# Optimization experiments

Measured on AMD Instinct MI355X. Metric: run time of the kernel, lower is better.

The kernel has to match this reference:

```python
import jax, jax.numpy as jnp
import numpy as np

B, C, H, W = 8, 256, 32, 32
N_HEAD, D_K, D_V, OUT_C = 8, 32, 32, 256


def _relative_indices(height, width):
    # idx[i, j] = (y_j - y_i + H) * W + (x_j - x_i + W), matching the torch loop
    ys, xs = np.meshgrid(np.arange(height), np.arange(width), indexing='ij')
    ys, xs = ys.reshape(-1), xs.reshape(-1)  # [L]
    rel_y = ys[None, :] - ys[:, None] + height  # [L, L]
    rel_x = xs[None, :] - xs[:, None] + width
    return jnp.asarray(rel_y * width + rel_x, dtype=jnp.int32)


def setup_inputs() -> dict:
    key = jax.random.key(0)
    ks = jax.random.split(key, 7)
    sc = lambda fan_in: 1.0 / np.sqrt(fan_in)
    table = ((2 * H - 1) * (2 * W - 1))  # 3969
    return {
        'x': jax.random.normal(ks[0], (B, C, H, W), jnp.float32),
        'Qw': jax.random.normal(ks[1], (C, N_HEAD * D_K), jnp.float32) * sc(C),
        'Kw': jax.random.normal(ks[2], (C, N_HEAD * D_K), jnp.float32) * sc(C),
        'Vw': jax.random.normal(ks[3], (C, N_HEAD * D_V), jnp.float32) * sc(C),
        'ffw': jax.random.normal(ks[4], (N_HEAD * D_V, OUT_C), jnp.float32) * sc(N_HEAD * D_V),
        'ffb': jax.random.normal(ks[5], (OUT_C,), jnp.float32) * 0.01,
        'rel_bias': jax.random.normal(ks[6], (N_HEAD, table), jnp.float32),
        'rel_idx': _relative_indices(H, W),  # [L, L] int32
    }


def reference(x, Qw, Kw, Vw, ffw, ffb, rel_bias, rel_idx):
    b, c, h_, w_ = x.shape
    L = h_ * w_
    nh = rel_bias.shape[0]
    dk = Qw.shape[1] // nh
    dv = Vw.shape[1] // nh
    xf = x.reshape(b, c, L).transpose(0, 2, 1)  # [b, L, c]
    q = (xf @ Qw).reshape(b, L, nh, dk).transpose(0, 2, 1, 3)  # [b, h, L, dk]
    k = (xf @ Kw).reshape(b, L, nh, dk).transpose(0, 2, 1, 3)
    v = (xf @ Vw).reshape(b, L, nh, dv).transpose(0, 2, 1, 3)
    bias = rel_bias[:, rel_idx]  # gather -> [h, L, L]
    sim = jnp.einsum('bhid,bhjd->bhij', q, k) + bias[None]  # no 1/sqrt(dk) in original
    attn = jax.nn.softmax(sim, axis=-1)  # dropout is identity in eval
    out = jnp.einsum('bhij,bhjd->bhid', attn, v)  # [b, h, L, dv]
    out = out.transpose(0, 2, 1, 3).reshape(b, L, nh * dv)
    out = out @ ffw + ffb  # [b, L, out_c]
    return out.transpose(0, 2, 1).reshape(b, -1, h_, w_)
```

## Files before the change

### kernel.cpp

```cpp
#include <hip/hip_runtime.h>
#include <math.h>


typedef unsigned short u16;
typedef __bf16 bf16;
typedef bf16 bf16x8 __attribute__((ext_vector_type(8)));
typedef bf16 bf16x4 __attribute__((ext_vector_type(4)));
typedef short s16x4 __attribute__((ext_vector_type(4)));
typedef float f32x4 __attribute__((ext_vector_type(4)));
typedef float f32x4u __attribute__((ext_vector_type(4), aligned(4)));
typedef u16 u16x8 __attribute__((ext_vector_type(8)));
typedef u16 u16x4 __attribute__((ext_vector_type(4)));

#define DEVI __device__ __forceinline__

DEVI u16 bfbits(float f) { return __builtin_bit_cast(u16, (bf16)f); }

DEVI void async_cp16(const u16* g, u16* l) {
    __builtin_amdgcn_global_load_lds((const __attribute__((address_space(1))) void*)g,
                                     (__attribute__((address_space(3))) void*)l, 16, 0, 0);
}

DEVI f32x4 pv_mfma(bf16x4 a, bf16x4 b, f32x4 c) {
#if __has_builtin(__builtin_amdgcn_mfma_f32_16x16x16bf16_1k)
    return __builtin_amdgcn_mfma_f32_16x16x16bf16_1k(
        __builtin_bit_cast(s16x4, a), __builtin_bit_cast(s16x4, b), c, 0, 0, 0);
#else
    asm("s_nop 1\n\tv_mfma_f32_16x16x16_bf16 %0, %1, %2, %0"
        : "+v"(c) : "v"(a), "v"(b));
    return c;
#endif
}

__global__ __launch_bounds__(256) void prep(const float* __restrict__ X,
                                            const float* __restrict__ Qw, const float* __restrict__ Kw,
                                            const float* __restrict__ Vw, const float* __restrict__ Fw,
                                            const float* __restrict__ RB,
                                            u16* __restrict__ XF, u16* __restrict__ WT,
                                            float* __restrict__ RBs) {
    __shared__ u16 t[64 * 65];
    const int blk = blockIdx.x, tid = threadIdx.x;
    if (blk < 576) {
        const float* src;
        int cbase, rbase, rows_total;
        u16* dst;
        if (blk < 512) {
            const int b = blk >> 6;
            cbase = (blk & 3) * 64; rbase = ((blk >> 2) & 15) * 64;
            src = X + (size_t)b * 256 * 1024; dst = XF + (size_t)b * 1024 * 256;
            rows_total = 1024;
        } else {
            const int t2 = blk - 512, wsel = t2 >> 4;
            cbase = (t2 & 3) * 64; rbase = ((t2 >> 2) & 3) * 64;
            src = wsel == 0 ? Qw : wsel == 1 ? Kw : wsel == 2 ? Vw : Fw;
            dst = WT + (size_t)wsel * 256 * 256;
            rows_total = 256;
        }
        const int w = tid >> 6, r = tid & 63;
#pragma unroll
        for (int i = 0; i < 16; i++) {
            const int c = w * 16 + i;
            t[c * 65 + r] = bfbits(src[(size_t)(cbase + c) * rows_total + rbase + r]);
        }
        __syncthreads();
#pragma unroll
        for (int i = 0; i < 2; i++) {
            const int idx = i * 256 + tid;
            const int r2 = idx >> 3, cg = idx & 7;
            u16x8 v;
#pragma unroll
            for (int j = 0; j < 8; j++) v[j] = t[(cg * 8 + j) * 65 + r2];
            *(u16x8*)&dst[(size_t)(rbase + r2) * 256 + cbase + cg * 8] = v;
        }
    } else {
        const int n = 8 * 3969;
        for (int i = (blk - 576) * 256 + tid; i < n; i += 32 * 256)
            RBs[i] = RB[i] * 1.44269504f;
    }
}

__global__ __launch_bounds__(256, 6) void gemm_fused(const u16* __restrict__ xf, const u16* __restrict__ wt,
                                                     u16* __restrict__ q, u16* __restrict__ kk,
                                                     u16* __restrict__ vt, const u16* __restrict__ ob,
                                                     float* __restrict__ outf, const float* __restrict__ ffb,
                                                     int base_mode) {
    __shared__ __align__(16) u16 lA[64 * 32];
    __shared__ __align__(16) u16 lB[64 * 32];
    const int tid = threadIdx.x;
    const int wave = tid >> 6, lane = tid & 63;
    const int quad = lane >> 4, l15 = lane & 15;

    int mode, mbase, nbase;
    const u16 *A, *Bt;
    if (base_mode == 2) {
        mode = 2; A = wt + 768 * 256; Bt = ob;
        mbase = (blockIdx.x & 3) * 64; nbase = (blockIdx.x >> 2) * 64;
    } else if (blockIdx.x < 1024) {
        mode = 0; A = xf; Bt = wt;
        mbase = (blockIdx.x >> 3) * 64; nbase = (blockIdx.x & 7) * 64;
    } else {
        mode = 1; A = wt + 512 * 256; Bt = xf;
        const int t = blockIdx.x - 1024;
        mbase = (t & 3) * 64; nbase = (t >> 2) * 64;
    }

    const int m0 = (wave >> 1) * 32, n0 = (wave & 1) * 32;
    const int srow = tid >> 2;
    const int sgcol = (lane & 3) ^ ((lane >> 3) & 3);
    const size_t arow = (size_t)(mbase + srow) * 256 + sgcol * 8;
    const size_t brow = (size_t)(nbase + srow) * 256 + sgcol * 8;
    const int kcol = ((quad ^ ((l15 >> 1) & 3))) * 8;

    f32x4 acc[2][2];
#pragma unroll
    for (int i = 0; i < 2; i++)
#pragma unroll
        for (int j = 0; j < 2; j++) acc[i][j] = f32x4{0.f, 0.f, 0.f, 0.f};

    for (int kb = 0; kb < 256; kb += 32) {
        __syncthreads();
        async_cp16(&A[arow + kb], &lA[wave * 512]);
        async_cp16(&Bt[brow + kb], &lB[wave * 512]);
        __syncthreads();
        bf16x8 af[2], bfr[2];
#pragma unroll
        for (int i = 0; i < 2; i++) af[i] = *(const bf16x8*)&lA[(m0 + i * 16 + l15) * 32 + kcol];
#pragma unroll
        for (int j = 0; j < 2; j++) bfr[j] = *(const bf16x8*)&lB[(n0 + j * 16 + l15) * 32 + kcol];
#pragma unroll
        for (int i = 0; i < 2; i++)
#pragma unroll
            for (int j = 0; j < 2; j++)
                acc[i][j] = __builtin_amdgcn_mfma_f32_16x16x32_bf16(af[i], bfr[j], acc[i][j], 0, 0, 0);
    }

#pragma unroll
    for (int i = 0; i < 2; i++) {
#pragma unroll
        for (int j = 0; j < 2; j++) {
#pragma unroll
            for (int r = 0; r < 4; r++) {
                const int gm = mbase + m0 + i * 16 + quad * 4 + r;
                const int gn = nbase + n0 + j * 16 + l15;
                float v = acc[i][j][r];
                if (mode == 0) {
                    const int b = gm >> 10, l = gm & 1023;
                    int n = gn;
                    u16* dst = q;
                    if (n >= 256) { n -= 256; dst = kk; }
                    else v *= 1.44269504f;
                    const int h = n >> 5, d = n & 31;
                    dst[(((size_t)(b * 8 + h) * 1024 + l) << 5) + d] = bfbits(v);
                } else if (mode == 1) {
                    const int h = gm >> 5, d = gm & 31;
                    const int b = gn >> 10, l = gn & 1023;
                    vt[(((size_t)(b * 8 + h) * 32 + d) << 10) + l] = bfbits(v);
                } else {
                    const int b = gn >> 10, l = gn & 1023;
                    outf[(((size_t)(b * 256 + gm)) << 10) + l] = v + ffb[gm];
                }
            }
        }
    }
}

__global__ __launch_bounds__(256, 4) void attn(const u16* __restrict__ Q, const u16* __restrict__ Kb,
                                               const u16* __restrict__ Vt, const float* __restrict__ RBs,
                                               u16* __restrict__ O) {
    __shared__ __align__(16) u16 kbuf[4][2][32 * 32];
    __shared__ __align__(16) u16 vbuf[4][2][32 * 32];
    const int tid = threadIdx.x;
    const int wave = tid >> 6, lane = tid & 63;
    const int quad = lane >> 4, l15 = lane & 15;
    const int blk = blockIdx.x;
    const int bh = ((blk >> 7) << 3) + (blk & 7);
    const int qt = (blk >> 3) & 15;
    const int b = bh >> 3, h = bh & 7;
    const int qbase = qt * 64 + wave * 16;
    const size_t bhL = (size_t)bh * 1024;

    const bf16x8 qf = *(const bf16x8*)&Q[(bhL + qbase + l15) * 32 + quad * 8];
    const float* brow0 = RBs + (size_t)h * 3969
                         + (32 - (qbase >> 5)) * 32 + 32 - (qbase & 31) - l15 + quad * 4;
    const int srow = lane >> 2;
    const int sgcol = (lane & 3) ^ ((lane >> 3) & 3);
    const u16* ksrc = &Kb[bhL * 32];
    const u16* vsrc_lo = &Vt[(((size_t)bh * 32) + srow) << 10];
    const u16* vsrc_hi = &Vt[(((size_t)bh * 32) + 16 + srow) << 10];

    float lsum = 0.f;
    f32x4 o_lo{0.f, 0.f, 0.f, 0.f}, o_hi{0.f, 0.f, 0.f, 0.f};

    const int swz = (l15 >> 1) & 3;
    const int kcol = (quad ^ swz) * 8;
    const int g0 = (2 * ((quad >> 1) ^ swz) + (quad & 1)) * 4;
    const int g1 = (2 * (((quad >> 1) + 2) ^ swz) + (quad & 1)) * 4;

#define STAGE(buf, c) do {                                                              \
        const int kb_ = (c) * 32;                                                       \
        async_cp16(ksrc + kb_ * 32 + srow * 32 + sgcol * 8, &kbuf[wave][buf][0]);       \
        async_cp16(ksrc + kb_ * 32 + 512 + srow * 32 + sgcol * 8, &kbuf[wave][buf][512]); \
        async_cp16(vsrc_lo + kb_ + sgcol * 8, &vbuf[wave][buf][0]);                     \
        async_cp16(vsrc_hi + kb_ + sgcol * 8, &vbuf[wave][buf][512]);                   \
    } while (0)

#define COMPUTE(cur, c) do {                                                              \
        const bf16x8 kf0 = *(const bf16x8*)&kbuf[wave][cur][l15 * 32 + kcol];             \
        const bf16x8 kf1 = *(const bf16x8*)&kbuf[wave][cur][(16 + l15) * 32 + kcol];      \
        const bf16x4 v00 = __builtin_bit_cast(bf16x4, *(const u16x4*)&vbuf[wave][cur][l15 * 32 + g0]); \
        const bf16x4 v10 = __builtin_bit_cast(bf16x4, *(const u16x4*)&vbuf[wave][cur][l15 * 32 + g1]); \
        const bf16x4 v01 = __builtin_bit_cast(bf16x4, *(const u16x4*)&vbuf[wave][cur][(16 + l15) * 32 + g0]); \
        const bf16x4 v11 = __builtin_bit_cast(bf16x4, *(const u16x4*)&vbuf[wave][cur][(16 + l15) * 32 + g1]); \
        const f32x4u b0 = *(const f32x4u*)(brow0 + (c) * 32);                             \
        const f32x4u b1 = *(const f32x4u*)(brow0 + (c) * 32 + 16);                        \
        const f32x4 z{0.f, 0.f, 0.f, 0.f};                                                \
        f32x4 s0 = __builtin_amdgcn_mfma_f32_16x16x32_bf16(kf0, qf, z, 0, 0, 0);          \
        f32x4 s1 = __builtin_amdgcn_mfma_f32_16x16x32_bf16(kf1, qf, z, 0, 0, 0);          \
        bf16x4 p0, p1;                                                                    \
        float ls0 = 0.f, ls1 = 0.f;                                                       \
        _Pragma("unroll")                                                                 \
        for (int r = 0; r < 4; r++) {                                                     \
            const float e0 = __builtin_amdgcn_exp2f(s0[r] + b0[r]);                       \
            const float e1 = __builtin_amdgcn_exp2f(s1[r] + b1[r]);                       \
            ls0 += e0; ls1 += e1;                                                         \
            p0[r] = (bf16)e0;                                                             \
            p1[r] = (bf16)e1;                                                             \
        }                                                                                 \
        lsum += ls0 + ls1;                                                                \
        o_lo = pv_mfma(p0, v00, o_lo);                                                    \
        o_hi = pv_mfma(p0, v01, o_hi);                                                    \
        o_lo = pv_mfma(p1, v10, o_lo);                                                    \
        o_hi = pv_mfma(p1, v11, o_hi);                                                    \
    } while (0)

#define WAIT4 asm volatile("s_waitcnt vmcnt(4)" ::: "memory")
#define WAIT0 asm volatile("s_waitcnt vmcnt(0)" ::: "memory")
#define DSDRAIN asm volatile("s_waitcnt lgkmcnt(0)" ::: "memory")

    STAGE(0, 0);
    STAGE(1, 1);
    for (int c = 0; c < 28; c += 2) {
        WAIT4; COMPUTE(0, c);     DSDRAIN; STAGE(0, c + 2);
        WAIT4; COMPUTE(1, c + 1); DSDRAIN; STAGE(1, c + 3);
    }
    WAIT4; COMPUTE(0, 28); DSDRAIN; STAGE(0, 30);
    WAIT4; COMPUTE(1, 29); DSDRAIN; STAGE(1, 31);
    WAIT4; COMPUTE(0, 30);
    WAIT0; COMPUTE(1, 31);
#undef STAGE
#undef COMPUTE
#undef WAIT4
#undef WAIT0
#undef DSDRAIN

    lsum += __shfl_xor(lsum, 16);
    lsum += __shfl_xor(lsum, 32);
#pragma unroll
    for (int r = 0; r < 4; r++) {
        const float inv = 1.f / __shfl(lsum, quad * 4 + r);
        const int i = qbase + quad * 4 + r;
        O[((size_t)(b * 1024 + i) * 256) + h * 32 + l15] = bfbits(o_lo[r] * inv);
        O[((size_t)(b * 1024 + i) * 256) + h * 32 + 16 + l15] = bfbits(o_hi[r] * inv);
    }
}

extern "C" void kernel_launch(void* const* d_in, const int* in_sizes, int n_in,
                              void* d_out, int out_size, void* d_ws, size_t ws_size,
                              hipStream_t stream) {
    const float* x   = (const float*)d_in[0];
    const float* Qw  = (const float*)d_in[1];
    const float* Kw  = (const float*)d_in[2];
    const float* Vw  = (const float*)d_in[3];
    const float* Fw  = (const float*)d_in[4];
    const float* ffb = (const float*)d_in[5];
    const float* RB  = (const float*)d_in[6];

    u16* ws = (u16*)d_ws;
    u16* xf = ws;
    u16* wt = xf + 2097152;
    u16* q  = wt + 262144;
    u16* kk = q  + 2097152;
    u16* vt = kk + 2097152;
    float* RBs = (float*)(vt + 2097152);
    u16* ob = xf;

    prep<<<dim3(608), 256, 0, stream>>>(x, Qw, Kw, Vw, Fw, RB, xf, wt, RBs);
    gemm_fused<<<dim3(1536), 256, 0, stream>>>(xf, wt, q, kk, vt, nullptr, nullptr, nullptr, 0);
    attn<<<dim3(1024), 256, 0, stream>>>(q, kk, vt, RBs, ob);
    gemm_fused<<<dim3(512), 256, 0, stream>>>(xf, wt, q, kk, vt, ob, (float*)d_out, ffb, 2);
}
```

Before: 124.6 us.

## Process two 16-row query tiles per wave to reuse staged K/V

Each wave in the attention kernel now handles 32 query rows instead of 16, so each K/V chunk staged into LDS serves two sets of score and PV MFMAs. This halves the grid and the total K/V global-to-LDS traffic per output, and the relative-bias rows for the second tile are shifted copies of the first, so one extra bias load covers them. In exchange it needs more registers per wave (launch bounds lowered to 2 blocks), gives fewer blocks to spread across CUs, and leaves less occupancy to hide latency.

```diff
diff --git a/kernel.cpp b/kernel.cpp
--- a/kernel.cpp
+++ b/kernel.cpp
@@ -164,7 +164,7 @@
     }
 }
 
-__global__ __launch_bounds__(256, 4) void attn(const u16* __restrict__ Q, const u16* __restrict__ Kb,
+__global__ __launch_bounds__(256, 2) void attn(const u16* __restrict__ Q, const u16* __restrict__ Kb,
                                                const u16* __restrict__ Vt, const float* __restrict__ RBs,
                                                u16* __restrict__ O) {
     __shared__ __align__(16) u16 kbuf[4][2][32 * 32];
@@ -173,23 +173,25 @@
     const int wave = tid >> 6, lane = tid & 63;
     const int quad = lane >> 4, l15 = lane & 15;
     const int blk = blockIdx.x;
-    const int bh = ((blk >> 7) << 3) + (blk & 7);
-    const int qt = (blk >> 3) & 15;
+    const int bh = ((blk >> 6) << 3) + (blk & 7);
+    const int qt = (blk >> 3) & 7;
     const int b = bh >> 3, h = bh & 7;
-    const int qbase = qt * 64 + wave * 16;
+    const int qbase = qt * 128 + wave * 32;
     const size_t bhL = (size_t)bh * 1024;
 
-    const bf16x8 qf = *(const bf16x8*)&Q[(bhL + qbase + l15) * 32 + quad * 8];
+    const bf16x8 qfA = *(const bf16x8*)&Q[(bhL + qbase + l15) * 32 + quad * 8];
+    const bf16x8 qfB = *(const bf16x8*)&Q[(bhL + qbase + 16 + l15) * 32 + quad * 8];
     const float* brow0 = RBs + (size_t)h * 3969
-                         + (32 - (qbase >> 5)) * 32 + 32 - (qbase & 31) - l15 + quad * 4;
+                         + (32 - (qbase >> 5)) * 32 + 32 - l15 + quad * 4;
     const int srow = lane >> 2;
     const int sgcol = (lane & 3) ^ ((lane >> 3) & 3);
     const u16* ksrc = &Kb[bhL * 32];
     const u16* vsrc_lo = &Vt[(((size_t)bh * 32) + srow) << 10];
     const u16* vsrc_hi = &Vt[(((size_t)bh * 32) + 16 + srow) << 10];
 
-    float lsum = 0.f;
-    f32x4 o_lo{0.f, 0.f, 0.f, 0.f}, o_hi{0.f, 0.f, 0.f, 0.f};
+    float lsumA = 0.f, lsumB = 0.f;
+    f32x4 oA_lo{0.f, 0.f, 0.f, 0.f}, oA_hi{0.f, 0.f, 0.f, 0.f};
+    f32x4 oB_lo{0.f, 0.f, 0.f, 0.f}, oB_hi{0.f, 0.f, 0.f, 0.f};
 
     const int swz = (l15 >> 1) & 3;
     const int kcol = (quad ^ swz) * 8;
@@ -211,26 +213,35 @@
         const bf16x4 v10 = __builtin_bit_cast(bf16x4, *(const u16x4*)&vbuf[wave][cur][l15 * 32 + g1]); \
         const bf16x4 v01 = __builtin_bit_cast(bf16x4, *(const u16x4*)&vbuf[wave][cur][(16 + l15) * 32 + g0]); \
         const bf16x4 v11 = __builtin_bit_cast(bf16x4, *(const u16x4*)&vbuf[wave][cur][(16 + l15) * 32 + g1]); \
+        const f32x4u bm = *(const f32x4u*)(brow0 + (c) * 32 - 16);                        \
         const f32x4u b0 = *(const f32x4u*)(brow0 + (c) * 32);                             \
         const f32x4u b1 = *(const f32x4u*)(brow0 + (c) * 32 + 16);                        \
         const f32x4 z{0.f, 0.f, 0.f, 0.f};                                                \
-        f32x4 s0 = __builtin_amdgcn_mfma_f32_16x16x32_bf16(kf0, qf, z, 0, 0, 0);          \
-        f32x4 s1 = __builtin_amdgcn_mfma_f32_16x16x32_bf16(kf1, qf, z, 0, 0, 0);          \
-        bf16x4 p0, p1;                                                                    \
-        float ls0 = 0.f, ls1 = 0.f;                                                       \
+        f32x4 s0A = __builtin_amdgcn_mfma_f32_16x16x32_bf16(kf0, qfA, z, 0, 0, 0);        \
+        f32x4 s1A = __builtin_amdgcn_mfma_f32_16x16x32_bf16(kf1, qfA, z, 0, 0, 0);        \
+        f32x4 s0B = __builtin_amdgcn_mfma_f32_16x16x32_bf16(kf0, qfB, z, 0, 0, 0);        \
+        f32x4 s1B = __builtin_amdgcn_mfma_f32_16x16x32_bf16(kf1, qfB, z, 0, 0, 0);        \
+        bf16x4 p0A, p1A, p0B, p1B;                                                        \
+        float lsA = 0.f, lsB = 0.f;                                                       \
         _Pragma("unroll")                                                                 \
         for (int r = 0; r < 4; r++) {                                                     \
-            const float e0 = __builtin_amdgcn_exp2f(s0[r] + b0[r]);                       \
-            const float e1 = __builtin_amdgcn_exp2f(s1[r] + b1[r]);                       \
-            ls0 += e0; ls1 += e1;                                                         \
-            p0[r] = (bf16)e0;                                                             \
-            p1[r] = (bf16)e1;                                                             \
+            const float e0A = __builtin_amdgcn_exp2f(s0A[r] + b0[r]);                     \
+            const float e1A = __builtin_amdgcn_exp2f(s1A[r] + b1[r]);                     \
+            const float e0B = __builtin_amdgcn_exp2f(s0B[r] + bm[r]);                     \
+            const float e1B = __builtin_amdgcn_exp2f(s1B[r] + b0[r]);                     \
+            lsA += e0A + e1A; lsB += e0B + e1B;                                           \
+            p0A[r] = (bf16)e0A; p1A[r] = (bf16)e1A;                                       \
+            p0B[r] = (bf16)e0B; p1B[r] = (bf16)e1B;                                       \
         }                                                                                 \
-        lsum += ls0 + ls1;                                                                \
-        o_lo = pv_mfma(p0, v00, o_lo);                                                    \
-        o_hi = pv_mfma(p0, v01, o_hi);                                                    \
-        o_lo = pv_mfma(p1, v10, o_lo);                                                    \
-        o_hi = pv_mfma(p1, v11, o_hi);                                                    \
+        lsumA += lsA; lsumB += lsB;                                                       \
+        oA_lo = pv_mfma(p0A, v00, oA_lo);                                                 \
+        oA_hi = pv_mfma(p0A, v01, oA_hi);                                                 \
+        oA_lo = pv_mfma(p1A, v10, oA_lo);                                                 \
+        oA_hi = pv_mfma(p1A, v11, oA_hi);                                                 \
+        oB_lo = pv_mfma(p0B, v00, oB_lo);                                                 \
+        oB_hi = pv_mfma(p0B, v01, oB_hi);                                                 \
+        oB_lo = pv_mfma(p1B, v10, oB_lo);                                                 \
+        oB_hi = pv_mfma(p1B, v11, oB_hi);                                                 \
     } while (0)
 
 #define WAIT4 asm volatile("s_waitcnt vmcnt(4)" ::: "memory")
@@ -253,14 +264,20 @@
 #undef WAIT0
 #undef DSDRAIN
 
-    lsum += __shfl_xor(lsum, 16);
-    lsum += __shfl_xor(lsum, 32);
+    lsumA += __shfl_xor(lsumA, 16);
+    lsumA += __shfl_xor(lsumA, 32);
+    lsumB += __shfl_xor(lsumB, 16);
+    lsumB += __shfl_xor(lsumB, 32);
 #pragma unroll
     for (int r = 0; r < 4; r++) {
-        const float inv = 1.f / __shfl(lsum, quad * 4 + r);
-        const int i = qbase + quad * 4 + r;
-        O[((size_t)(b * 1024 + i) * 256) + h * 32 + l15] = bfbits(o_lo[r] * inv);
-        O[((size_t)(b * 1024 + i) * 256) + h * 32 + 16 + l15] = bfbits(o_hi[r] * inv);
+        const float invA = 1.f / __shfl(lsumA, quad * 4 + r);
+        const float invB = 1.f / __shfl(lsumB, quad * 4 + r);
+        const int iA = qbase + quad * 4 + r;
+        const int iB = iA + 16;
+        O[((size_t)(b * 1024 + iA) * 256) + h * 32 + l15] = bfbits(oA_lo[r] * invA);
+        O[((size_t)(b * 1024 + iA) * 256) + h * 32 + 16 + l15] = bfbits(oA_hi[r] * invA);
+        O[((size_t)(b * 1024 + iB) * 256) + h * 32 + l15] = bfbits(oB_lo[r] * invB);
+        O[((size_t)(b * 1024 + iB) * 256) + h * 32 + 16 + l15] = bfbits(oB_hi[r] * invB);
     }
 }
 
@@ -286,6 +303,6 @@
 
     prep<<<dim3(608), 256, 0, stream>>>(x, Qw, Kw, Vw, Fw, RB, xf, wt, RBs);
     gemm_fused<<<dim3(1536), 256, 0, stream>>>(xf, wt, q, kk, vt, nullptr, nullptr, nullptr, 0);
-    attn<<<dim3(1024), 256, 0, stream>>>(q, kk, vt, RBs, ob);
+    attn<<<dim3(512), 256, 0, stream>>>(q, kk, vt, RBs, ob);
     gemm_fused<<<dim3(512), 256, 0, stream>>>(xf, wt, q, kk, vt, ob, (float*)d_out, ffb, 2);
 }
```

Result: faster. 118.3 us (-5.0%).
